# Kernel tuning notes

Measured on AMD Instinct MI355X. Metric: run time of the kernel, lower is better.

## Reference

```python
import jax, jax.numpy as jnp
import numpy as np

NUM_EMBEDDINGS = 8192
EMBEDDING_DIM = 512
COMMITMENT_COST = 0.25
DECAY = 0.99
EPSILON = 1e-05


def _l2_normalize(x, axis=-1, eps=1e-12):
    # matches torch.nn.functional.normalize (p=2)
    n = jnp.sqrt(jnp.sum(x * x, axis=axis, keepdims=True))
    return x / jnp.maximum(n, eps)


def setup_inputs() -> dict:
    key = jax.random.key(0)
    k1, k2, k3 = jax.random.split(key, 3)
    inputs = jax.random.normal(k1, (8, 4096, EMBEDDING_DIM), dtype=jnp.float32)
    embedding = jax.random.normal(k2, (NUM_EMBEDDINGS, EMBEDDING_DIM), dtype=jnp.float32) * 0.01
    ema_cluster_size = jnp.ones((NUM_EMBEDDINGS,), dtype=jnp.float32)
    ema_w = jax.random.normal(k3, (NUM_EMBEDDINGS, EMBEDDING_DIM), dtype=jnp.float32) * 0.01
    return {"inputs": inputs, "embedding": embedding,
            "ema_cluster_size": ema_cluster_size, "ema_w": ema_w}


def reference(inputs, embedding, ema_cluster_size, ema_w):
    K, D = NUM_EMBEDDINGS, EMBEDDING_DIM
    flat = _l2_normalize(inputs.reshape(-1, D))           # [N, D]
    emb_n = _l2_normalize(embedding)                       # [K, D] (in-place normalize in torch)

    # cosine distance: 1 - flat @ emb^T  -> argmin
    distances = 1.0 - jnp.matmul(flat, emb_n.T)            # [N, K]
    idx = jnp.argmin(distances, axis=1)                    # [N]

    # one-hot @ codebook == gather
    quantized = jnp.take(emb_n, idx, axis=0).reshape(inputs.shape)

    # EMA codebook update (training branch), scatter-encode via segment_sum
    counts = jax.ops.segment_sum(jnp.ones_like(idx, dtype=flat.dtype), idx,
                                 num_segments=K)           # [K]
    new_cs = ema_cluster_size * DECAY + (1.0 - DECAY) * counts
    n = jnp.sum(new_cs)
    new_cs = (new_cs + EPSILON) / (n + K * EPSILON) * n
    dw = jax.ops.segment_sum(flat, idx, num_segments=K)    # [K, D] == one_hot^T @ flat
    new_ema_w = ema_w * DECAY + (1.0 - DECAY) * dw
    new_embedding = new_ema_w / jnp.clip(new_cs, EPSILON, None)[:, None]

    e_latent_loss = jnp.mean((jax.lax.stop_gradient(quantized) - inputs) ** 2)
    loss = COMMITMENT_COST * e_latent_loss

    quantized_st = inputs + jax.lax.stop_gradient(quantized - inputs)
    encoding_indices = idx.reshape(inputs.shape[:-1])
    return (quantized_st, loss, encoding_indices, new_cs, new_ema_w, new_embedding)
```

## Files before the change

kernel.cpp:

```cpp
#include <hip/hip_runtime.h>
#include <math.h>

#define NROWS 32768
#define DIM   512
#define KCODE 8192
#define DECAYF 0.99f
#define OMDF   0.01f
#define EPSF   1e-5f
#define COMMITF 0.25f
#define MARGIN 8e-4f

typedef _Float16 half8 __attribute__((ext_vector_type(8)));
typedef _Float16 half4v __attribute__((ext_vector_type(4)));
typedef _Float16 half2v __attribute__((ext_vector_type(2)));
typedef float floatx16 __attribute__((ext_vector_type(16)));


__device__ __forceinline__ float block_sum_256(float v) {
    __shared__ float sm[4];
    int lane = threadIdx.x & 63, wave = threadIdx.x >> 6;
    #pragma unroll
    for (int off = 32; off; off >>= 1) v += __shfl_down(v, off);
    if (lane == 0) sm[wave] = v;
    __syncthreads();
    if (threadIdx.x == 0) v = sm[0] + sm[1] + sm[2] + sm[3];
    return v;
}

__global__ void k_rownorm_inv(const float* __restrict__ x, float* __restrict__ inv) {
    int wave = threadIdx.x >> 6;
    int lane = threadIdx.x & 63;
    int row = blockIdx.x * 4 + wave;
    const float* p = x + (size_t)row * DIM;
    float4 f1 = *(const float4*)&p[lane * 4];
    float4 f2 = *(const float4*)&p[256 + lane * 4];
    float s = f1.x*f1.x + f1.y*f1.y + f1.z*f1.z + f1.w*f1.w
            + f2.x*f2.x + f2.y*f2.y + f2.z*f2.z + f2.w*f2.w;
    #pragma unroll
    for (int off = 32; off; off >>= 1) s += __shfl_down(s, off);
    if (lane == 0) inv[row] = 1.0f / fmaxf(sqrtf(s), 1e-12f);
}

__global__ void k_split(const float* __restrict__ src, const float* __restrict__ inv,
                        _Float16* __restrict__ hi, _Float16* __restrict__ lo) {
    const int i4 = (blockIdx.x * 256 + threadIdx.x) * 4;
    const float iv = inv[i4 >> 9];
    const float4 v = *(const float4*)&src[i4];
    float n0 = v.x * iv, n1 = v.y * iv, n2 = v.z * iv, n3 = v.w * iv;
    _Float16 h0 = (_Float16)n0, h1 = (_Float16)n1, h2 = (_Float16)n2, h3 = (_Float16)n3;
    half4v hv = {h0, h1, h2, h3};
    *(half4v*)&hi[i4] = hv;
    half4v lv = {(_Float16)((n0 - (float)h0) * 4096.f),
                 (_Float16)((n1 - (float)h1) * 4096.f),
                 (_Float16)((n2 - (float)h2) * 4096.f),
                 (_Float16)((n3 - (float)h3) * 4096.f)};
    *(half4v*)&lo[i4] = lv;
}

__device__ __forceinline__ void gld16(const _Float16* g, _Float16* l) {
    __builtin_amdgcn_global_load_lds(
        (const __attribute__((address_space(1))) void*)g,
        (__attribute__((address_space(3))) void*)l, 16, 0, 0);
}

__device__ __forceinline__ void top2_upd(float v, int i, float& v1, int& i1, float& v2) {
    if (v > v1) { v2 = v1; v1 = v; i1 = i; }
    else        { v2 = fmaxf(v2, v); }
}

__device__ __forceinline__ void stage_step(const _Float16* __restrict__ Xh,
                                           const _Float16* __restrict__ Eh,
                                           _Float16* dst, int split, int rowBase,
                                           int ss, int w, int rg, int colOff) {
    const int ntB = split * 4096 + (ss >> 4) * 256;
    const int kts = (ss & 15) << 5;
    #pragma unroll
    for (int j = 0; j < 6; ++j) {
        const int m = w * 6 + j;
        const int r = m * 16 + rg;
        const _Float16* src = (m < 16)
            ? (Eh + (size_t)(ntB + r) * DIM + (kts + colOff))
            : (Xh + (size_t)(rowBase + (r - 256)) * DIM + (kts + colOff));
        gld16(src, dst + m * 512);
    }
}

__launch_bounds__(256, 2)
__global__ void k_hi(const _Float16* __restrict__ Xh, const _Float16* __restrict__ Eh,
                     float* __restrict__ sV1, float* __restrict__ sV2,
                     unsigned short* __restrict__ sI1) {
    __shared__ __align__(16) _Float16 lds[3 * 12288];
    __shared__ float mV[128][2], mV2[128][2];
    __shared__ int   mI[128][2];

    const int tid  = threadIdx.x;
    const int w    = tid >> 6;
    const int lane = tid & 63;
    const int wc = w & 1, wr = w >> 1;
    const int c = lane & 31, h = lane >> 5;
    const int rowBase = blockIdx.x * 128;
    const int split   = blockIdx.y;

    const int rg   = lane >> 2;
    const int slot = lane & 3;
    const int colOff = (slot ^ ((rg ^ (rg >> 2)) & 3)) * 8;

    const int Pc = (c ^ (c >> 2)) & 3;
    const int rowB = wr * 64 + c;

    float v1a = -1e30f, v2a = -1e30f, v1b = -1e30f, v2b = -1e30f;
    int i1a = 0, i1b = 0;

    stage_step(Xh, Eh, &lds[0],     split, rowBase, 0, w, rg, colOff);
    stage_step(Xh, Eh, &lds[12288], split, rowBase, 1, w, rg, colOff);
    int br = 0, bs = 2;

    for (int nt = 0; nt < 16; ++nt) {
        const int ntBase = split * 4096 + nt * 256;
        floatx16 acc[4][2];
        #pragma unroll
        for (int i = 0; i < 4; ++i)
            #pragma unroll
            for (int j = 0; j < 2; ++j)
                #pragma unroll
                for (int r = 0; r < 16; ++r) acc[i][j][r] = 0.f;

        for (int kt16 = 0; kt16 < 16; ++kt16) {
            const int s = nt * 16 + kt16;
            asm volatile("s_waitcnt vmcnt(6)" ::: "memory");
            __builtin_amdgcn_sched_barrier(0);
            __builtin_amdgcn_s_barrier();
            __builtin_amdgcn_sched_barrier(0);
            stage_step(Xh, Eh, &lds[bs * 12288], split, rowBase,
                       (s + 2) & 255, w, rg, colOff);
            __builtin_amdgcn_sched_barrier(0);
            const _Float16* B = &lds[br * 12288];
            #pragma unroll
            for (int ks = 0; ks < 2; ++ks) {
                const int so = (((ks << 1) + h) ^ Pc) << 3;
                half8 a0 = *(const half8*)&B[(wc * 128 +  0 + c) * 32 + so];
                half8 a1 = *(const half8*)&B[(wc * 128 + 32 + c) * 32 + so];
                half8 a2 = *(const half8*)&B[(wc * 128 + 64 + c) * 32 + so];
                half8 a3 = *(const half8*)&B[(wc * 128 + 96 + c) * 32 + so];
                half8 b0 = *(const half8*)&B[8192 + (rowB) * 32 + so];
                half8 b1 = *(const half8*)&B[8192 + (rowB + 32) * 32 + so];
                __builtin_amdgcn_s_setprio(1);
                acc[0][0] = __builtin_amdgcn_mfma_f32_32x32x16_f16(a0, b0, acc[0][0], 0, 0, 0);
                acc[1][0] = __builtin_amdgcn_mfma_f32_32x32x16_f16(a1, b0, acc[1][0], 0, 0, 0);
                acc[2][0] = __builtin_amdgcn_mfma_f32_32x32x16_f16(a2, b0, acc[2][0], 0, 0, 0);
                acc[3][0] = __builtin_amdgcn_mfma_f32_32x32x16_f16(a3, b0, acc[3][0], 0, 0, 0);
                acc[0][1] = __builtin_amdgcn_mfma_f32_32x32x16_f16(a0, b1, acc[0][1], 0, 0, 0);
                acc[1][1] = __builtin_amdgcn_mfma_f32_32x32x16_f16(a1, b1, acc[1][1], 0, 0, 0);
                acc[2][1] = __builtin_amdgcn_mfma_f32_32x32x16_f16(a2, b1, acc[2][1], 0, 0, 0);
                acc[3][1] = __builtin_amdgcn_mfma_f32_32x32x16_f16(a3, b1, acc[3][1], 0, 0, 0);
                __builtin_amdgcn_s_setprio(0);
            }
            br = (br == 2) ? 0 : br + 1;
            bs = (bs == 2) ? 0 : bs + 1;
        }
        #pragma unroll
        for (int r = 0; r < 16; ++r) {
            const int codeSub = (r & 3) + ((r >> 2) << 3) + (h << 2);
            #pragma unroll
            for (int i = 0; i < 4; ++i) {
                const int code = ntBase + wc * 128 + i * 32 + codeSub;
                top2_upd(acc[i][0][r], code, v1a, i1a, v2a);
                top2_upd(acc[i][1][r], code, v1b, i1b, v2b);
            }
        }
    }

    {
        float ov1 = __shfl_xor(v1a, 32); int oi1 = __shfl_xor(i1a, 32); float ov2 = __shfl_xor(v2a, 32);
        if (ov1 > v1a) { v2a = fmaxf(v1a, ov2); v1a = ov1; i1a = oi1; }
        else if (ov1 == v1a) { v2a = v1a; if (oi1 < i1a) i1a = oi1; }
        else { v2a = fmaxf(v2a, ov1); }
        ov1 = __shfl_xor(v1b, 32); oi1 = __shfl_xor(i1b, 32); ov2 = __shfl_xor(v2b, 32);
        if (ov1 > v1b) { v2b = fmaxf(v1b, ov2); v1b = ov1; i1b = oi1; }
        else if (ov1 == v1b) { v2b = v1b; if (oi1 < i1b) i1b = oi1; }
        else { v2b = fmaxf(v2b, ov1); }
    }
    if (h == 0) {
        mV[rowB][wc] = v1a; mV2[rowB][wc] = v2a; mI[rowB][wc] = i1a;
        mV[rowB + 32][wc] = v1b; mV2[rowB + 32][wc] = v2b; mI[rowB + 32][wc] = i1b;
    }
    __syncthreads();
    if (tid < 128) {
        float v1 = mV[tid][0], v2 = mV2[tid][0]; int i1 = mI[tid][0];
        float ov1 = mV[tid][1], ov2 = mV2[tid][1]; int oi1 = mI[tid][1];
        if (ov1 > v1) { v2 = fmaxf(v1, ov2); v1 = ov1; i1 = oi1; }
        else if (ov1 == v1) { v2 = v1; if (oi1 < i1) i1 = oi1; }
        else { v2 = fmaxf(v2, ov1); }
        const int n = rowBase + tid;
        sV1[split * NROWS + n] = v1;
        sV2[split * NROWS + n] = v2;
        sI1[split * NROWS + n] = (unsigned short)i1;
    }
}

__global__ void k_top2_merge(const float* __restrict__ sV1, const float* __restrict__ sV2,
                             const unsigned short* __restrict__ sI1,
                             float* __restrict__ outIdx, int* __restrict__ list,
                             int* __restrict__ flagCnt) {
    const int n = blockIdx.x * 256 + threadIdx.x;
    float a1 = sV1[n], a2 = sV2[n]; int ai = sI1[n];
    float b1 = sV1[NROWS + n], b2 = sV2[NROWS + n]; int bi = sI1[NROWS + n];
    float best, run; int bidx;
    if (b1 > a1) { best = b1; bidx = bi; run = fmaxf(a1, b2); }
    else         { best = a1; bidx = ai; run = fmaxf(a2, b1); }
    outIdx[n] = (float)bidx;
    if (best - run < MARGIN) {
        int p = atomicAdd(flagCnt, 1);
        list[p] = n;
    }
}

__device__ __forceinline__ unsigned long long encodeKey(float v, int idx) {
    unsigned u = __float_as_uint(v);
    u = (u & 0x80000000u) ? ~u : (u | 0x80000000u);
    return ((unsigned long long)u << 32) | (unsigned)(0xFFFFFFFFu - (unsigned)idx);
}

__launch_bounds__(256, 2)
__global__ void k_rescore(const _Float16* __restrict__ Xh, const _Float16* __restrict__ Xl,
                          const _Float16* __restrict__ Eh, const _Float16* __restrict__ El,
                          const int* __restrict__ list, const int* __restrict__ flagCnt,
                          unsigned long long* __restrict__ rkey) {
    const int cnt = *flagCnt;
    const int t = blockIdx.x & 255;
    const int s = blockIdx.x >> 8;
    if (t * 128 >= cnt) return;

    __shared__ __align__(16) _Float16 lds[32768];
    __shared__ float mV[128][2];
    __shared__ int   mI[128][2];

    const int tid  = threadIdx.x;
    const int w    = tid >> 6;
    const int lane = tid & 63;
    const int wc = w & 1, wr = w >> 1;
    const int c = lane & 31, h = lane >> 5;
    const int sr = lane >> 3;
    const int sg = (lane & 7) ^ (sr & 7);
    const int rowA = wc * 64 + c;
    const int rowB = wr * 64 + c;
    const int cx = c & 7;

    int rows_j[4];
    #pragma unroll
    for (int j = 0; j < 4; ++j) {
        const int slot = t * 128 + w * 32 + j * 8 + sr;
        rows_j[j] = (slot < cnt) ? list[slot] : 0;
    }

    float best0 = -1e30f, best1 = -1e30f;
    int bi0 = 0, bi1 = 0;
    const float SC = 1.0f / 4096.0f;

    for (int nt = 0; nt < 4; ++nt) {
        const int ntBase = s * 512 + nt * 128;

        floatx16 accH00, accH01, accH10, accH11, accC00, accC01, accC10, accC11;
        #pragma unroll
        for (int r = 0; r < 16; ++r) {
            accH00[r] = 0.f; accH01[r] = 0.f; accH10[r] = 0.f; accH11[r] = 0.f;
            accC00[r] = 0.f; accC01[r] = 0.f; accC10[r] = 0.f; accC11[r] = 0.f;
        }

        for (int chunk = 0; chunk < 8; ++chunk) {
            const int kt = chunk * 64;
            #pragma unroll
            for (int j = 0; j < 4; ++j) {
                const int rl = w * 32 + j * 8 + sr;
                const size_t gE = (size_t)(ntBase + rl) * DIM + kt + sg * 8;
                const size_t gX = (size_t)rows_j[j] * DIM + kt + sg * 8;
                _Float16* dBase = &lds[(w * 32 + j * 8) * 64];
                gld16(Eh + gE, dBase);
                gld16(El + gE, dBase + 8192);
                gld16(Xh + gX, dBase + 16384);
                gld16(Xl + gX, dBase + 24576);
            }
            __syncthreads();
            #pragma unroll
            for (int ks = 0; ks < 4; ++ks) {
                const int so = ((ks * 2 + h) ^ cx) * 8;
                const half8 ah0 = *(const half8*)&lds[rowA * 64 + so];
                const half8 ah1 = *(const half8*)&lds[(rowA + 32) * 64 + so];
                const half8 al0 = *(const half8*)&lds[8192 + rowA * 64 + so];
                const half8 al1 = *(const half8*)&lds[8192 + (rowA + 32) * 64 + so];
                const half8 bh0 = *(const half8*)&lds[16384 + rowB * 64 + so];
                const half8 bh1 = *(const half8*)&lds[16384 + (rowB + 32) * 64 + so];
                const half8 bl0 = *(const half8*)&lds[24576 + rowB * 64 + so];
                const half8 bl1 = *(const half8*)&lds[24576 + (rowB + 32) * 64 + so];

                accH00 = __builtin_amdgcn_mfma_f32_32x32x16_f16(ah0, bh0, accH00, 0, 0, 0);
                accC00 = __builtin_amdgcn_mfma_f32_32x32x16_f16(ah0, bl0, accC00, 0, 0, 0);
                accC00 = __builtin_amdgcn_mfma_f32_32x32x16_f16(al0, bh0, accC00, 0, 0, 0);

                accH01 = __builtin_amdgcn_mfma_f32_32x32x16_f16(ah0, bh1, accH01, 0, 0, 0);
                accC01 = __builtin_amdgcn_mfma_f32_32x32x16_f16(ah0, bl1, accC01, 0, 0, 0);
                accC01 = __builtin_amdgcn_mfma_f32_32x32x16_f16(al0, bh1, accC01, 0, 0, 0);

                accH10 = __builtin_amdgcn_mfma_f32_32x32x16_f16(ah1, bh0, accH10, 0, 0, 0);
                accC10 = __builtin_amdgcn_mfma_f32_32x32x16_f16(ah1, bl0, accC10, 0, 0, 0);
                accC10 = __builtin_amdgcn_mfma_f32_32x32x16_f16(al1, bh0, accC10, 0, 0, 0);

                accH11 = __builtin_amdgcn_mfma_f32_32x32x16_f16(ah1, bh1, accH11, 0, 0, 0);
                accC11 = __builtin_amdgcn_mfma_f32_32x32x16_f16(ah1, bl1, accC11, 0, 0, 0);
                accC11 = __builtin_amdgcn_mfma_f32_32x32x16_f16(al1, bh1, accC11, 0, 0, 0);
            }
            __syncthreads();
        }

        #pragma unroll
        for (int r = 0; r < 16; ++r) {
            const int codeSub = (r & 3) + ((r >> 2) << 3) + (h << 2);
            const int code0 = ntBase + wc * 64 + codeSub;
            const int code1 = code0 + 32;
            float v;
            v = fmaf(accC00[r], SC, accH00[r]);
            if (v > best0 || (v == best0 && code0 < bi0)) { best0 = v; bi0 = code0; }
            v = fmaf(accC10[r], SC, accH10[r]);
            if (v > best0 || (v == best0 && code1 < bi0)) { best0 = v; bi0 = code1; }
            v = fmaf(accC01[r], SC, accH01[r]);
            if (v > best1 || (v == best1 && code0 < bi1)) { best1 = v; bi1 = code0; }
            v = fmaf(accC11[r], SC, accH11[r]);
            if (v > best1 || (v == best1 && code1 < bi1)) { best1 = v; bi1 = code1; }
        }
    }

    {
        float ov = __shfl_xor(best0, 32); int oi = __shfl_xor(bi0, 32);
        if (ov > best0 || (ov == best0 && oi < bi0)) { best0 = ov; bi0 = oi; }
        ov = __shfl_xor(best1, 32); oi = __shfl_xor(bi1, 32);
        if (ov > best1 || (ov == best1 && oi < bi1)) { best1 = ov; bi1 = oi; }
    }
    if (h == 0) {
        mV[rowB][wc] = best0;      mI[rowB][wc] = bi0;
        mV[rowB + 32][wc] = best1; mI[rowB + 32][wc] = bi1;
    }
    __syncthreads();
    if (tid < 128) {
        const int slot = t * 128 + tid;
        if (slot < cnt) {
            float v0 = mV[tid][0]; int i0 = mI[tid][0];
            float v1 = mV[tid][1]; int i1 = mI[tid][1];
            float bv; int bidx;
            if (v1 > v0 || (v1 == v0 && i1 < i0)) { bv = v1; bidx = i1; }
            else                                  { bv = v0; bidx = i0; }
            atomicMax(&rkey[list[slot]], encodeKey(bv, bidx));
        }
    }
}

__global__ void k_rescore_merge(const unsigned long long* __restrict__ rkey,
                                const int* __restrict__ list, const int* __restrict__ flagCnt,
                                float* __restrict__ outIdx) {
    const int slot = blockIdx.x * 256 + threadIdx.x;
    if (slot < *flagCnt) {
        const int row = list[slot];
        const unsigned long long key = rkey[row];
        const int code = (int)(0xFFFFFFFFu - (unsigned)(key & 0xFFFFFFFFull));
        outIdx[row] = (float)code;
    }
}

__global__ void k_hist(const float* __restrict__ outIdx, int* __restrict__ cntI) {
    const int n = blockIdx.x * 256 + threadIdx.x;
    atomicAdd(&cntI[(int)outIdx[n]], 1);
}

__global__ void k_gather_loss(const float* __restrict__ X, const _Float16* __restrict__ Eh,
                              const _Float16* __restrict__ El, const float* __restrict__ outIdx,
                              float* __restrict__ qst, float* __restrict__ lossAcc) {
    const float SC = 1.0f / 4096.0f;
    float acc = 0.f;
    #pragma unroll
    for (int it = 0; it < 8; ++it) {
        const int e = (it * 2048 + blockIdx.x) * 256 + threadIdx.x;
        const int row = e >> 7;
        const int col = (e & 127) * 4;
        const int k = (int)outIdx[row];
        const float4 x = ((const float4*)X)[e];
        const half4v eh = *(const half4v*)&Eh[(size_t)k * DIM + col];
        const half4v el = *(const half4v*)&El[(size_t)k * DIM + col];
        const float q0 = (float)eh.x + (float)el.x * SC;
        const float q1 = (float)eh.y + (float)el.y * SC;
        const float q2 = (float)eh.z + (float)el.z * SC;
        const float q3 = (float)eh.w + (float)el.w * SC;
        const float d0 = q0 - x.x, d1 = q1 - x.y, d2 = q2 - x.z, d3 = q3 - x.w;
        float4 o; o.x = x.x + d0; o.y = x.y + d1; o.z = x.z + d2; o.w = x.w + d3;
        ((float4*)qst)[e] = o;
        acc += d0 * d0 + d1 * d1 + d2 * d2 + d3 * d3;
    }
    const float ls = block_sum_256(acc);
    if (threadIdx.x == 0) atomicAdd(lossAcc, ls);
}

__global__ void k_cs_pre(const float* __restrict__ emacs, const int* __restrict__ cntI,
                         float* __restrict__ pre, float* __restrict__ nsum) {
    const int k = blockIdx.x * 256 + threadIdx.x;
    float p = emacs[k] * DECAYF + OMDF * (float)cntI[k];
    pre[k] = p;
    float s = block_sum_256(p);
    if (threadIdx.x == 0) atomicAdd(nsum, s);
}

__global__ void k_cs_final(const float* __restrict__ pre, const float* __restrict__ nsum,
                           float* __restrict__ outCS, float* __restrict__ csfin,
                           const float* __restrict__ lossAcc, float* __restrict__ outLoss) {
    const int k = blockIdx.x * 256 + threadIdx.x;
    float n = *nsum;
    float c = (pre[k] + EPSF) / (n + (float)KCODE * EPSF) * n;
    outCS[k] = c;
    csfin[k] = c;
    if (k == 0) *outLoss = COMMITF * (*lossAcc) / (float)(NROWS * DIM);
}

__global__ void k_scan(const int* __restrict__ cntI, int* __restrict__ offs) {
    __shared__ int ps[1024];
    const int t = threadIdx.x;
    int loc[8], pref[8], s = 0;
    #pragma unroll
    for (int j = 0; j < 8; ++j) { loc[j] = cntI[t * 8 + j]; pref[j] = s; s += loc[j]; }
    ps[t] = s;
    __syncthreads();
    for (int d = 1; d < 1024; d <<= 1) {
        int x = (t >= d) ? ps[t - d] : 0;
        __syncthreads();
        ps[t] += x;
        __syncthreads();
    }
    const int base = ps[t] - s;
    #pragma unroll
    for (int j = 0; j < 8; ++j) offs[t * 8 + j] = base + pref[j];
}

__global__ void k_bin(const float* __restrict__ outIdx, const int* __restrict__ offs,
                      int* __restrict__ cursor, int* __restrict__ perm) {
    const int n = blockIdx.x * 256 + threadIdx.x;
    const int k = (int)outIdx[n];
    const int pos = offs[k] + atomicAdd(&cursor[k], 1);
    perm[pos] = n;
}

__global__ void k_dw_fused(const float* __restrict__ X, const float* __restrict__ inv_in,
                           const int* __restrict__ perm, const int* __restrict__ offs,
                           const int* __restrict__ cntI, const float* __restrict__ emaw,
                           const float* __restrict__ csfin,
                           float* __restrict__ outW, float* __restrict__ outE) {
    const int k = blockIdx.x;
    const int t = threadIdx.x;
    const int c = cntI[k];
    const int base = offs[k];
    float a0 = 0.f, a1 = 0.f;
    for (int i = 0; i < c; ++i) {
        const int row = perm[base + i];
        const float iv = inv_in[row];
        const float2 x = *(const float2*)&X[(size_t)row * DIM + t * 2];
        a0 = fmaf(x.x, iv, a0);
        a1 = fmaf(x.y, iv, a1);
    }
    const float2 w2 = *(const float2*)&emaw[(size_t)k * DIM + t * 2];
    const float w0 = w2.x * DECAYF + OMDF * a0;
    const float w1 = w2.y * DECAYF + OMDF * a1;
    float2 ow; ow.x = w0; ow.y = w1;
    *(float2*)&outW[(size_t)k * DIM + t * 2] = ow;
    const float cs = fmaxf(csfin[k], EPSF);
    float2 oe; oe.x = w0 / cs; oe.y = w1 / cs;
    *(float2*)&outE[(size_t)k * DIM + t * 2] = oe;
}

extern "C" void kernel_launch(void* const* d_in, const int* in_sizes, int n_in,
                              void* d_out, int out_size, void* d_ws, size_t ws_size,
                              hipStream_t stream) {
    const float* inputs    = (const float*)d_in[0];
    const float* embedding = (const float*)d_in[1];
    const float* emacs     = (const float*)d_in[2];
    const float* emaw      = (const float*)d_in[3];
    float* out = (float*)d_out;
    float* ws  = (float*)d_ws;

    float* inv_in  = ws;
    float* sV1     = ws + 32768;
    float* sV2     = ws + 98304;
    unsigned short* sI1 = (unsigned short*)(ws + 163840);
    int*   list    = (int*)(ws + 196608);
    int*   flagCnt = (int*)(ws + 229376);
    float* inv_emb = ws + 229440;
    _Float16* Xh   = (_Float16*)(ws + 229440);
    _Float16* Xl   = (_Float16*)(ws + 8618048);
    _Float16* Eh   = (_Float16*)(ws + 17006656);
    _Float16* El   = (_Float16*)(ws + 19103808);
    unsigned long long* rkey = (unsigned long long*)(ws + 32768);
    int*   cntI    = (int*)(ws + 98304);
    int*   cursor  = (int*)(ws + 106496);
    float* lossAcc = ws + 114688;
    float* nsum    = ws + 114689;
    float* pre     = ws + 114692;
    float* csfin   = ws + 122884;
    int*   offs    = (int*)(ws + 131076);
    int*   perm    = (int*)(ws + 139268);

    float* outQst  = out;
    float* outLoss = out + 16777216;
    float* outIdx  = out + 16777217;
    float* outCS   = out + 16809985;
    float* outW    = out + 16818177;
    float* outE    = out + 21012481;

    hipMemsetAsync(flagCnt, 0, sizeof(int), stream);
    k_rownorm_inv<<<NROWS / 4, 256, 0, stream>>>(inputs, inv_in);
    k_rownorm_inv<<<KCODE / 4, 256, 0, stream>>>(embedding, inv_emb);
    k_split<<<KCODE * DIM / 1024, 256, 0, stream>>>(embedding, inv_emb, Eh, El);
    k_split<<<NROWS * DIM / 1024, 256, 0, stream>>>(inputs, inv_in, Xh, Xl);
    k_hi<<<dim3(NROWS / 128, 2), 256, 0, stream>>>(Xh, Eh, sV1, sV2, sI1);
    k_top2_merge<<<NROWS / 256, 256, 0, stream>>>(sV1, sV2, sI1, outIdx, list, flagCnt);
    hipMemsetAsync(ws + 32768, 0, (size_t)81922 * sizeof(float), stream);
    k_rescore<<<4096, 256, 0, stream>>>(Xh, Xl, Eh, El, list, flagCnt, rkey);
    k_rescore_merge<<<NROWS / 256, 256, 0, stream>>>(rkey, list, flagCnt, outIdx);
    k_hist<<<NROWS / 256, 256, 0, stream>>>(outIdx, cntI);
    k_gather_loss<<<2048, 256, 0, stream>>>(inputs, Eh, El, outIdx, outQst, lossAcc);
    k_cs_pre<<<KCODE / 256, 256, 0, stream>>>(emacs, cntI, pre, nsum);
    k_cs_final<<<KCODE / 256, 256, 0, stream>>>(pre, nsum, outCS, csfin, lossAcc, outLoss);
    k_scan<<<1, 1024, 0, stream>>>(cntI, offs);
    k_bin<<<NROWS / 256, 256, 0, stream>>>(outIdx, offs, cursor, perm);
    k_dw_fused<<<KCODE, 256, 0, stream>>>(inputs, inv_in, perm, offs, cntI, emaw, csfin,
                                          outW, outE);
}
```

Measured before the change: 728.3 us.

## Enlarge k_hi block tile to 256 rows with 8 waves and 4-stage pipeline

Changes the main fp16 similarity GEMM kernel from 256-thread blocks covering 128 input rows to 512-thread blocks covering 256 rows. Each stage now loads 256 codes and 256 rows into a 4-deep LDS ring instead of a 3-deep one, and the k loop is fully unrolled. The goal is to raise data reuse per loaded codebook tile and hide more global latency. The cost is larger LDS use (128KB per block) and fewer resident blocks, which may reduce occupancy.

```diff
diff --git a/kernel.cpp b/kernel.cpp
--- a/kernel.cpp
+++ b/kernel.cpp
@@ -71,49 +71,46 @@
 __device__ __forceinline__ void stage_step(const _Float16* __restrict__ Xh,
                                            const _Float16* __restrict__ Eh,
                                            _Float16* dst, int split, int rowBase,
-                                           int ss, int w, int rg, int colOff) {
-    const int ntB = split * 4096 + (ss >> 4) * 256;
-    const int kts = (ss & 15) << 5;
-    #pragma unroll
-    for (int j = 0; j < 6; ++j) {
-        const int m = w * 6 + j;
-        const int r = m * 16 + rg;
-        const _Float16* src = (m < 16)
-            ? (Eh + (size_t)(ntB + r) * DIM + (kts + colOff))
-            : (Xh + (size_t)(rowBase + (r - 256)) * DIM + (kts + colOff));
-        gld16(src, dst + m * 512);
-    }
-}
-
-__launch_bounds__(256, 2)
+                                           int S, int r0, int ldsOff, int colOff) {
+    const int ntB = split * 4096 + (S >> 4) * 256;
+    const int col = ((S & 15) << 5) + colOff;
+    gld16(Eh + (size_t)(ntB + r0)           * DIM + col, dst + ldsOff);
+    gld16(Eh + (size_t)(ntB + 128 + r0)     * DIM + col, dst + 4096 + ldsOff);
+    gld16(Xh + (size_t)(rowBase + r0)       * DIM + col, dst + 8192 + ldsOff);
+    gld16(Xh + (size_t)(rowBase + 128 + r0) * DIM + col, dst + 12288 + ldsOff);
+}
+
+__launch_bounds__(512, 2)
 __global__ void k_hi(const _Float16* __restrict__ Xh, const _Float16* __restrict__ Eh,
                      float* __restrict__ sV1, float* __restrict__ sV2,
                      unsigned short* __restrict__ sI1) {
-    __shared__ __align__(16) _Float16 lds[3 * 12288];
-    __shared__ float mV[128][2], mV2[128][2];
-    __shared__ int   mI[128][2];
+    __shared__ __align__(16) _Float16 lds[4 * 16384];
+    __shared__ float mV[256][2], mV2[256][2];
+    __shared__ int   mI[256][2];
 
     const int tid  = threadIdx.x;
     const int w    = tid >> 6;
     const int lane = tid & 63;
-    const int wc = w & 1, wr = w >> 1;
+    const int wc  = w & 1;
+    const int wrr = w >> 1;
     const int c = lane & 31, h = lane >> 5;
-    const int rowBase = blockIdx.x * 128;
+    const int rowBase = blockIdx.x * 256;
     const int split   = blockIdx.y;
 
-    const int rg   = lane >> 2;
-    const int slot = lane & 3;
-    const int colOff = (slot ^ ((rg ^ (rg >> 2)) & 3)) * 8;
+    const int r0   = tid >> 2;
+    const int slot = tid & 3;
+    const int Ps   = ((tid >> 2) ^ (tid >> 4)) & 3;
+    const int colOff = (slot ^ Ps) * 8;
+    const int ldsOff = r0 * 32 + slot * 8;
 
     const int Pc = (c ^ (c >> 2)) & 3;
-    const int rowB = wr * 64 + c;
 
     float v1a = -1e30f, v2a = -1e30f, v1b = -1e30f, v2b = -1e30f;
     int i1a = 0, i1b = 0;
 
-    stage_step(Xh, Eh, &lds[0],     split, rowBase, 0, w, rg, colOff);
-    stage_step(Xh, Eh, &lds[12288], split, rowBase, 1, w, rg, colOff);
-    int br = 0, bs = 2;
+    stage_step(Xh, Eh, &lds[0],     split, rowBase, 0, r0, ldsOff, colOff);
+    stage_step(Xh, Eh, &lds[16384], split, rowBase, 1, r0, ldsOff, colOff);
+    stage_step(Xh, Eh, &lds[32768], split, rowBase, 2, r0, ldsOff, colOff);
 
     for (int nt = 0; nt < 16; ++nt) {
         const int ntBase = split * 4096 + nt * 256;
@@ -125,16 +122,15 @@
                 #pragma unroll
                 for (int r = 0; r < 16; ++r) acc[i][j][r] = 0.f;
 
-        for (int kt16 = 0; kt16 < 16; ++kt16) {
-            const int s = nt * 16 + kt16;
-            asm volatile("s_waitcnt vmcnt(6)" ::: "memory");
-            __builtin_amdgcn_sched_barrier(0);
+        #pragma unroll
+        for (int k = 0; k < 16; ++k) {
+            const int S = nt * 16 + k;
+            asm volatile("s_waitcnt vmcnt(8) lgkmcnt(0)" ::: "memory");
             __builtin_amdgcn_s_barrier();
-            __builtin_amdgcn_sched_barrier(0);
-            stage_step(Xh, Eh, &lds[bs * 12288], split, rowBase,
-                       (s + 2) & 255, w, rg, colOff);
-            __builtin_amdgcn_sched_barrier(0);
-            const _Float16* B = &lds[br * 12288];
+            asm volatile("" ::: "memory");
+            stage_step(Xh, Eh, &lds[((k + 3) & 3) * 16384], split, rowBase,
+                       (S + 3) & 255, r0, ldsOff, colOff);
+            const _Float16* B = &lds[(k & 3) * 16384];
             #pragma unroll
             for (int ks = 0; ks < 2; ++ks) {
                 const int so = (((ks << 1) + h) ^ Pc) << 3;
@@ -142,8 +138,8 @@
                 half8 a1 = *(const half8*)&B[(wc * 128 + 32 + c) * 32 + so];
                 half8 a2 = *(const half8*)&B[(wc * 128 + 64 + c) * 32 + so];
                 half8 a3 = *(const half8*)&B[(wc * 128 + 96 + c) * 32 + so];
-                half8 b0 = *(const half8*)&B[8192 + (rowB) * 32 + so];
-                half8 b1 = *(const half8*)&B[8192 + (rowB + 32) * 32 + so];
+                half8 b0 = *(const half8*)&B[8192 + (wrr * 64 +  0 + c) * 32 + so];
+                half8 b1 = *(const half8*)&B[8192 + (wrr * 64 + 32 + c) * 32 + so];
                 __builtin_amdgcn_s_setprio(1);
                 acc[0][0] = __builtin_amdgcn_mfma_f32_32x32x16_f16(a0, b0, acc[0][0], 0, 0, 0);
                 acc[1][0] = __builtin_amdgcn_mfma_f32_32x32x16_f16(a1, b0, acc[1][0], 0, 0, 0);
@@ -155,8 +151,6 @@
                 acc[3][1] = __builtin_amdgcn_mfma_f32_32x32x16_f16(a3, b1, acc[3][1], 0, 0, 0);
                 __builtin_amdgcn_s_setprio(0);
             }
-            br = (br == 2) ? 0 : br + 1;
-            bs = (bs == 2) ? 0 : bs + 1;
         }
         #pragma unroll
         for (int r = 0; r < 16; ++r) {
@@ -181,11 +175,12 @@
         else { v2b = fmaxf(v2b, ov1); }
     }
     if (h == 0) {
-        mV[rowB][wc] = v1a; mV2[rowB][wc] = v2a; mI[rowB][wc] = i1a;
-        mV[rowB + 32][wc] = v1b; mV2[rowB + 32][wc] = v2b; mI[rowB + 32][wc] = i1b;
+        const int rA = wrr * 64 + c;
+        mV[rA][wc] = v1a; mV2[rA][wc] = v2a; mI[rA][wc] = i1a;
+        mV[rA + 32][wc] = v1b; mV2[rA + 32][wc] = v2b; mI[rA + 32][wc] = i1b;
     }
     __syncthreads();
-    if (tid < 128) {
+    if (tid < 256) {
         float v1 = mV[tid][0], v2 = mV2[tid][0]; int i1 = mI[tid][0];
         float ov1 = mV[tid][1], ov2 = mV2[tid][1]; int oi1 = mI[tid][1];
         if (ov1 > v1) { v2 = fmaxf(v1, ov2); v1 = ov1; i1 = oi1; }
@@ -514,7 +509,7 @@
     k_rownorm_inv<<<KCODE / 4, 256, 0, stream>>>(embedding, inv_emb);
     k_split<<<KCODE * DIM / 1024, 256, 0, stream>>>(embedding, inv_emb, Eh, El);
     k_split<<<NROWS * DIM / 1024, 256, 0, stream>>>(inputs, inv_in, Xh, Xl);
-    k_hi<<<dim3(NROWS / 128, 2), 256, 0, stream>>>(Xh, Eh, sV1, sV2, sI1);
+    k_hi<<<dim3(NROWS / 256, 2), 512, 0, stream>>>(Xh, Eh, sV1, sV2, sI1);
     k_top2_merge<<<NROWS / 256, 256, 0, stream>>>(sV1, sV2, sI1, outIdx, list, flagCnt);
     hipMemsetAsync(ws + 32768, 0, (size_t)81922 * sizeof(float), stream);
     k_rescore<<<4096, 256, 0, stream>>>(Xh, Xl, Eh, El, list, flagCnt, rkey);
```

Result: faster. 681.4 us (-6.4%).
